# Performance work log

Measured on AMD Instinct MI355X. Metric: run time of the kernel, lower is better.

Reference implementation:

```python
import jax, jax.numpy as jnp
import numpy as np

LAMB = 0.1
SIZE_AVERAGE = True


def setup_inputs() -> dict:
    key = jax.random.key(0)
    k1, k2 = jax.random.split(key)
    N, D = 8192, 4096
    inp = jax.random.normal(k1, (N, D), dtype=jnp.float32)
    target = jax.random.normal(k2, (N, D), dtype=jnp.float32)
    return {"input": inp, "target": target}


def _drae_loss(inp, target, lamb=LAMB, size_average=SIZE_AVERAGE):
    # Per-sample squared reconstruction error: Err[n] = sum_d (inp - target)^2
    err = (inp - target).reshape(inp.shape[0], -1)
    Err = jnp.sum(err * err, axis=1)                      # [N]
    N = Err.shape[0]
    sErr = jnp.sort(Err)                                  # ascending

    # Prefix sums replace the original O(N^2) Python scan.
    cs = jnp.cumsum(sErr)                                 # [N]
    cs2 = jnp.cumsum(sErr * sErr)                         # [N]
    total, total2 = cs[-1], cs2[-1]
    nf = jnp.asarray(N, sErr.dtype)
    allMean = total / nf
    Sb = total2 - nf * allMean * allMean                  # sum (e - allMean)^2

    # Candidate splits: inlier count k = 1..N-1 (loop index i = k-1).
    k = jnp.arange(1, N, dtype=sErr.dtype)                # [N-1]
    csk, cs2k = cs[:-1], cs2[:-1]
    Sw1 = cs2k - csk * csk / k                            # within-inlier scatter
    Sw2 = (total2 - cs2k) - (total - csk) ** 2 / (nf - k) # within-outlier scatter
    obj = (Sw1 + Sw2) / Sb                                # Fisher-style ratio

    i = jnp.argmin(obj)                                   # first min, like strict '<'
    optObj = obj[i]
    T = (i + 1).astype(sErr.dtype)                        # inlier count
    inlier_sum = cs[i]

    out = inlier_sum / T if size_average else inlier_sum
    return out + lamb * optObj


def reference(input, target):
    return _drae_loss(input, target)
```

## Files before the change

kernel.cpp:

```cpp
#include <hip/hip_runtime.h>

#define NROWS 8192
#define NCOLS 4096
#define LAMB  0.1
#define NBUCK 2048

typedef unsigned int u32;
typedef unsigned long long u64;

__global__ __launch_bounds__(256) void rowerr_kernel(const float* __restrict__ inp,
                                                     const float* __restrict__ tgt,
                                                     float* __restrict__ err) {
    const int row = blockIdx.x;
    const float4* a = reinterpret_cast<const float4*>(inp + (size_t)row * NCOLS);
    const float4* b = reinterpret_cast<const float4*>(tgt + (size_t)row * NCOLS);
    const int t = threadIdx.x;

    float acc = 0.f;
#pragma unroll
    for (int c = 0; c < 4; ++c) {
        float4 va = a[t + c * 256];
        float4 vb = b[t + c * 256];
        float dx = va.x - vb.x;
        float dy = va.y - vb.y;
        float dz = va.z - vb.z;
        float dw = va.w - vb.w;
        acc += dx * dx + dy * dy + dz * dz + dw * dw;
    }

#pragma unroll
    for (int off = 32; off > 0; off >>= 1) acc += __shfl_down(acc, off, 64);

    __shared__ float ws[4];
    const int lane = t & 63, wv = t >> 6;
    if (lane == 0) ws[wv] = acc;
    __syncthreads();
    if (t == 0) err[row] = ws[0] + ws[1] + ws[2] + ws[3];
}

__device__ __forceinline__ double fastrcp(double x) {
    double r = (double)(1.0f / (float)x);
    r = r * (2.0 - x * r);
    r = r * (2.0 - x * r);
    return r;
}

__global__ __launch_bounds__(1024) void drae_kernel(const float* __restrict__ err,
                                                    float* __restrict__ out) {
    const int N = NROWS;
    __shared__ u32 bufB[NROWS];
    __shared__ u32 hist[NBUCK];
    __shared__ u32 base2[NBUCK];
    __shared__ u32 sMin[16], sMax[16], saux[16];
    __shared__ double auxX[16], auxT2[16], redH[16], redCs[16];
    __shared__ int    redIdx[16];

    const int tid  = threadIdx.x;
    const int lane = tid & 63, wv = tid >> 6;

    u32 bits[8];
    {
        const float4* e4 = reinterpret_cast<const float4*>(err);
        const float4 f0 = e4[tid];
        const float4 f1 = e4[tid + 1024];
        bits[0] = __float_as_uint(f0.x);
        bits[1] = __float_as_uint(f0.y);
        bits[2] = __float_as_uint(f0.z);
        bits[3] = __float_as_uint(f0.w);
        bits[4] = __float_as_uint(f1.x);
        bits[5] = __float_as_uint(f1.y);
        bits[6] = __float_as_uint(f1.z);
        bits[7] = __float_as_uint(f1.w);
    }
    u32 mn = 0xFFFFFFFFu, mx = 0u;
#pragma unroll
    for (int k = 0; k < 8; ++k) { mn = min(mn, bits[k]); mx = max(mx, bits[k]); }
#pragma unroll
    for (int off = 32; off > 0; off >>= 1) {
        mn = min(mn, (u32)__shfl_xor((int)mn, off, 64));
        mx = max(mx, (u32)__shfl_xor((int)mx, off, 64));
    }
    if (lane == 0) { sMin[wv] = mn; sMax[wv] = mx; }

    hist[tid] = 0;
    hist[tid + 1024] = 0;
    __syncthreads();

    u32 minb = sMin[0], maxb = sMax[0];
#pragma unroll
    for (int w = 1; w < 16; ++w) { minb = min(minb, sMin[w]); maxb = max(maxb, sMax[w]); }
    const u32 range = maxb - minb;
    const int nbits = 32 - __clz(range | 1u);
    const int shift = (nbits > 11) ? (nbits - 11) : 0;

    u32 bk[8];
#pragma unroll
    for (int k = 0; k < 8; ++k) {
        bits[k] -= minb;
        bk[k] = bits[k] >> shift;
        atomicAdd(&hist[bk[k]], 1u);
    }
    __syncthreads();

    const u32 c0 = hist[2 * tid], c1 = hist[2 * tid + 1];
    const u32 tsum = c0 + c1;
    u32 incl = tsum;
#pragma unroll
    for (int off = 1; off < 64; off <<= 1) {
        const u32 t = __shfl_up(incl, off, 64);
        if (lane >= off) incl += t;
    }
    if (lane == 63) saux[wv] = incl;
    __syncthreads();
    u32 add = 0;
#pragma unroll
    for (int w = 0; w < 16; ++w) if (w < wv) add += saux[w];
    const u32 excl = add + incl - tsum;
    base2[2 * tid] = excl;           base2[2 * tid + 1] = excl + c0;
    hist[2 * tid]  = excl;           hist[2 * tid + 1]  = excl + c0;
    __syncthreads();

    u32 myq[8];
#pragma unroll
    for (int k = 0; k < 8; ++k) {
        const u32 p = atomicAdd(&hist[bk[k]], 1u);
        myq[k] = p - base2[bk[k]];
        bufB[p] = bits[k];
    }
    __syncthreads();

    u32 pos[8];
#pragma unroll
    for (int k = 0; k < 8; ++k) {
        const u32 s = base2[bk[k]];
        const u32 e = hist[bk[k]];
        const u32 ki = bits[k];
        u32 r = 0;
        for (u32 q = 0; q < e - s; ++q) {
            const u32 v = bufB[s + q];
            r += (v < ki || (v == ki && q < myq[k])) ? 1u : 0u;
        }
        pos[k] = s + r;
    }
    __syncthreads();

#pragma unroll
    for (int k = 0; k < 8; ++k) bufB[pos[k]] = bits[k];
    __syncthreads();

    float v[8];
#pragma unroll
    for (int r = 0; r < 8; ++r) v[r] = __uint_as_float(bufB[(tid << 3) + r] + minb);

    double sx = 0.0, sx2 = 0.0;
#pragma unroll
    for (int r = 0; r < 8; ++r) {
        sx  += (double)v[r];
        sx2 += (double)v[r] * (double)v[r];
    }

    double ix = sx;
#pragma unroll
    for (int off = 1; off < 64; off <<= 1) {
        double t1 = __shfl_up(ix, off, 64);
        if (lane >= off) ix += t1;
    }
    double t2 = sx2;
#pragma unroll
    for (int off = 32; off > 0; off >>= 1) t2 += __shfl_xor(t2, off, 64);

    if (lane == 63) auxX[wv]  = ix;
    if (lane == 0)  auxT2[wv] = t2;
    __syncthreads();

    double wOff1 = 0.0, total1 = 0.0, total2 = 0.0;
#pragma unroll
    for (int w = 0; w < 16; ++w) {
        const double a1 = auxX[w];
        if (w < wv) wOff1 += a1;
        total1 += a1;
        total2 += auxT2[w];
    }
    const double exc1 = wOff1 + (ix - sx);
    const double nf = (double)N;

    double run1 = exc1;
    double bestH = -1e300, bestCs = 0.0;
    int bestIdx = N;
#pragma unroll
    for (int r = 0; r < 8; ++r) {
        const int idx = (tid << 3) + r;
        run1 += (double)v[r];
        if (idx < N - 1) {
            const double kf  = (double)(idx + 1);
            const double rem = total1 - run1;
            const double h   = run1 * run1 * fastrcp(kf) +
                               rem  * rem  * fastrcp(nf - kf);
            if (h > bestH) { bestH = h; bestIdx = idx; bestCs = run1; }
        }
    }

#pragma unroll
    for (int off = 32; off > 0; off >>= 1) {
        const double oH   = __shfl_down(bestH, off, 64);
        const int    oIdx = __shfl_down(bestIdx, off, 64);
        const double oCs  = __shfl_down(bestCs, off, 64);
        if (oH > bestH || (oH == bestH && oIdx < bestIdx)) {
            bestH = oH; bestIdx = oIdx; bestCs = oCs;
        }
    }
    if (lane == 0) { redH[wv] = bestH; redIdx[wv] = bestIdx; redCs[wv] = bestCs; }
    __syncthreads();

    if (tid == 0) {
        double bH = redH[0], bCs = redCs[0];
        int bIdx = redIdx[0];
        for (int w = 1; w < 16; ++w) {
            if (redH[w] > bH || (redH[w] == bH && redIdx[w] < bIdx)) {
                bH = redH[w]; bIdx = redIdx[w]; bCs = redCs[w];
            }
        }
        const double Sb     = total2 - total1 * total1 / nf;
        const double optObj = (total2 - bH) / Sb;
        const double T      = (double)(bIdx + 1);
        out[0] = (float)(bCs / T + LAMB * optObj);
    }
}

extern "C" void kernel_launch(void* const* d_in, const int* in_sizes, int n_in,
                              void* d_out, int out_size, void* d_ws, size_t ws_size,
                              hipStream_t stream) {
    const float* inp = (const float*)d_in[0];
    const float* tgt = (const float*)d_in[1];
    float* errbuf = (float*)d_ws;

    rowerr_kernel<<<NROWS, 256, 0, stream>>>(inp, tgt, errbuf);
    drae_kernel<<<1, 1024, 0, stream>>>(errbuf, (float*)d_out);
}
```

Baseline: 69.54 us.

## Fuse row-error and sort/select kernels via last-block atomic counter

Merges the per-row squared-error kernel and the single-block sort/prefix/argmin kernel into one launch of 1024 blocks, each computing 8 rows. An atomic counter elects the last finishing block to run the selection stage, which removes the second kernel launch and its dependency gap. In exchange it adds a memset launch for the counter and makes every block carry a large shared-memory footprint (the 32KB sort buffer plus histograms), which may reduce occupancy during the bandwidth-bound phase.

```diff
diff --git a/kernel.cpp b/kernel.cpp
--- a/kernel.cpp
+++ b/kernel.cpp
@@ -4,39 +4,10 @@
 #define NCOLS 4096
 #define LAMB  0.1
 #define NBUCK 2048
+#define NBLK  1024
 
 typedef unsigned int u32;
 typedef unsigned long long u64;
-
-__global__ __launch_bounds__(256) void rowerr_kernel(const float* __restrict__ inp,
-                                                     const float* __restrict__ tgt,
-                                                     float* __restrict__ err) {
-    const int row = blockIdx.x;
-    const float4* a = reinterpret_cast<const float4*>(inp + (size_t)row * NCOLS);
-    const float4* b = reinterpret_cast<const float4*>(tgt + (size_t)row * NCOLS);
-    const int t = threadIdx.x;
-
-    float acc = 0.f;
-#pragma unroll
-    for (int c = 0; c < 4; ++c) {
-        float4 va = a[t + c * 256];
-        float4 vb = b[t + c * 256];
-        float dx = va.x - vb.x;
-        float dy = va.y - vb.y;
-        float dz = va.z - vb.z;
-        float dw = va.w - vb.w;
-        acc += dx * dx + dy * dy + dz * dz + dw * dw;
-    }
-
-#pragma unroll
-    for (int off = 32; off > 0; off >>= 1) acc += __shfl_down(acc, off, 64);
-
-    __shared__ float ws[4];
-    const int lane = t & 63, wv = t >> 6;
-    if (lane == 0) ws[wv] = acc;
-    __syncthreads();
-    if (t == 0) err[row] = ws[0] + ws[1] + ws[2] + ws[3];
-}
 
 __device__ __forceinline__ double fastrcp(double x) {
     double r = (double)(1.0f / (float)x);
@@ -45,36 +16,78 @@
     return r;
 }
 
-__global__ __launch_bounds__(1024) void drae_kernel(const float* __restrict__ err,
-                                                    float* __restrict__ out) {
+__global__ __launch_bounds__(1024) void fused_kernel(const float* __restrict__ inp,
+                                                     const float* __restrict__ tgt,
+                                                     float* err, u32* counter,
+                                                     float* __restrict__ out) {
     const int N = NROWS;
     __shared__ u32 bufB[NROWS];
     __shared__ u32 hist[NBUCK];
     __shared__ u32 base2[NBUCK];
+    __shared__ float ws[32];
     __shared__ u32 sMin[16], sMax[16], saux[16];
     __shared__ double auxX[16], auxT2[16], redH[16], redCs[16];
     __shared__ int    redIdx[16];
+    __shared__ int    amLast;
 
     const int tid  = threadIdx.x;
     const int lane = tid & 63, wv = tid >> 6;
+    const int gid  = tid >> 8;
+    const int t256 = tid & 255;
+    const int wvg  = (tid >> 6) & 3;
+
+    const int row0 = blockIdx.x * 8 + gid * 2;
+    float accr[2];
+#pragma unroll
+    for (int rr = 0; rr < 2; ++rr) {
+        const float4* a = reinterpret_cast<const float4*>(inp + (size_t)(row0 + rr) * NCOLS);
+        const float4* b = reinterpret_cast<const float4*>(tgt + (size_t)(row0 + rr) * NCOLS);
+        float acc = 0.f;
+#pragma unroll
+        for (int c = 0; c < 4; ++c) {
+            const float4 va = a[t256 + c * 256];
+            const float4 vb = b[t256 + c * 256];
+            const float dx = va.x - vb.x;
+            const float dy = va.y - vb.y;
+            const float dz = va.z - vb.z;
+            const float dw = va.w - vb.w;
+            acc += dx * dx + dy * dy + dz * dz + dw * dw;
+        }
+#pragma unroll
+        for (int off = 32; off > 0; off >>= 1) acc += __shfl_down(acc, off, 64);
+        accr[rr] = acc;
+    }
+    if (lane == 0) {
+        ws[gid * 8 + wvg]     = accr[0];
+        ws[gid * 8 + 4 + wvg] = accr[1];
+    }
+    __syncthreads();
+    if (t256 == 0) {
+        const float v0 = (ws[gid*8+0] + ws[gid*8+1]) + (ws[gid*8+2] + ws[gid*8+3]);
+        const float v1 = (ws[gid*8+4] + ws[gid*8+5]) + (ws[gid*8+6] + ws[gid*8+7]);
+        __hip_atomic_store(&err[row0],     v0, __ATOMIC_RELAXED, __HIP_MEMORY_SCOPE_AGENT);
+        __hip_atomic_store(&err[row0 + 1], v1, __ATOMIC_RELAXED, __HIP_MEMORY_SCOPE_AGENT);
+    }
+
+    __syncthreads();
+    if (tid == 0) {
+        const u32 old = __hip_atomic_fetch_add(counter, 1u, __ATOMIC_ACQ_REL,
+                                               __HIP_MEMORY_SCOPE_AGENT);
+        amLast = (old == (u32)(NBLK - 1));
+    }
+    __syncthreads();
+    if (!amLast) return;
 
     u32 bits[8];
-    {
-        const float4* e4 = reinterpret_cast<const float4*>(err);
-        const float4 f0 = e4[tid];
-        const float4 f1 = e4[tid + 1024];
-        bits[0] = __float_as_uint(f0.x);
-        bits[1] = __float_as_uint(f0.y);
-        bits[2] = __float_as_uint(f0.z);
-        bits[3] = __float_as_uint(f0.w);
-        bits[4] = __float_as_uint(f1.x);
-        bits[5] = __float_as_uint(f1.y);
-        bits[6] = __float_as_uint(f1.z);
-        bits[7] = __float_as_uint(f1.w);
-    }
     u32 mn = 0xFFFFFFFFu, mx = 0u;
 #pragma unroll
-    for (int k = 0; k < 8; ++k) { mn = min(mn, bits[k]); mx = max(mx, bits[k]); }
+    for (int k = 0; k < 8; ++k) {
+        const float v = __hip_atomic_load(&err[tid + k * 1024], __ATOMIC_RELAXED,
+                                          __HIP_MEMORY_SCOPE_AGENT);
+        bits[k] = __float_as_uint(v);
+        mn = min(mn, bits[k]);
+        mx = max(mx, bits[k]);
+    }
 #pragma unroll
     for (int off = 32; off > 0; off >>= 1) {
         mn = min(mn, (u32)__shfl_xor((int)mn, off, 64));
@@ -232,8 +245,10 @@
                               hipStream_t stream) {
     const float* inp = (const float*)d_in[0];
     const float* tgt = (const float*)d_in[1];
-    float* errbuf = (float*)d_ws;
-
-    rowerr_kernel<<<NROWS, 256, 0, stream>>>(inp, tgt, errbuf);
-    drae_kernel<<<1, 1024, 0, stream>>>(errbuf, (float*)d_out);
+    float* errbuf  = (float*)d_ws;
+    u32*   counter = (u32*)((char*)d_ws + NROWS * 4);
+
+    hipMemsetAsync(counter, 0, 4, stream);
+    fused_kernel<<<NBLK, 1024, 0, stream>>>(inp, tgt, errbuf, counter,
+                                            (float*)d_out);
 }
```

After: 88.07 us. 1.27x slower.
